# Kernel optimization log

Hardware: AMD Instinct MI355X
Metric: run time of the kernel (lower is better)

## Reference

```python
import jax, jax.numpy as jnp
import numpy as np

NUM_FIELDS = 16
EMBED = 256
BATCH = 2048
NUM_PAIRS = NUM_FIELDS * (NUM_FIELDS - 1) // 2  # 120


def setup_inputs() -> dict:
    key = jax.random.key(0)
    k1, k2, k3 = jax.random.split(key, 3)
    emb_inputs = jax.random.normal(k1, (BATCH, NUM_FIELDS, EMBED), dtype=jnp.float32)
    bound = 1.0 / np.sqrt(NUM_PAIRS)  # torch: 1/sqrt(weight.size(0)) = 1/sqrt(in_features)
    weight = jax.random.uniform(k2, (NUM_PAIRS, EMBED, EMBED), dtype=jnp.float32,
                                minval=-bound, maxval=bound)
    bias = jax.random.uniform(k3, (NUM_PAIRS, EMBED), dtype=jnp.float32,
                              minval=-bound, maxval=bound)
    return {"emb_inputs": emb_inputs, "weight": weight, "bias": bias}


def reference(emb_inputs, weight, bias):
    # Pair indices (i, j) with i < j over fields
    row_idx, col_idx = np.triu_indices(NUM_FIELDS, k=1)  # each length NUM_PAIRS
    p = emb_inputs[:, row_idx]  # (B, P, E)
    q = emb_inputs[:, col_idx]  # (B, P, E)
    # FieldEachTypeBilinear: (p @ W_p) * q + b_p, per-pair weight W_p (E, E)
    out = jnp.einsum('bpe,pef->bpf', p, weight) * q + bias  # (B, P, E)
    return out
```

## Files before the change

### kernel.cpp

```cpp
#include <hip/hip_runtime.h>
#include <hip/hip_bf16.h>
#include <stdint.h>

#define BATCH   2048
#define NF      16
#define EMBED   256
#define NPAIRS  120
#define OUTROW  (NPAIRS*EMBED)
#define EMBROW  (NF*EMBED)

typedef __attribute__((ext_vector_type(8))) __bf16 bf16x8;
typedef __attribute__((ext_vector_type(4))) float  f32x4;

typedef __attribute__((address_space(3))) void       lds_void;
typedef const __attribute__((address_space(1))) void g_void;

__device__ __forceinline__ unsigned short f2bf(float f) {
    unsigned u = __float_as_uint(f);
    u += 0x7FFF + ((u >> 16) & 1);
    return (unsigned short)(u >> 16);
}

__device__ __forceinline__ void pair_rc(int p, int& r, int& c) {
    int rr = 0, base = 0;
    while (p >= base + (NF - 1 - rr)) { base += NF - 1 - rr; ++rr; }
    r = rr; c = rr + 1 + (p - base);
}

__global__ __launch_bounds__(256) void emb_permute(const float* __restrict__ emb,
                                                   unsigned short* __restrict__ embp) {
    __shared__ float tile[64][65];
    const int b0 = blockIdx.x * 64;
    const int e0 = blockIdx.y * 64;
    const int f  = blockIdx.z;
    const int t  = threadIdx.x;
#pragma unroll
    for (int rnd = 0; rnd < 4; ++rnd) {
        int bl = rnd * 16 + (t >> 4);
        int el = (t & 15) * 4;
        const float4 v = *(const float4*)(emb + (size_t)(b0 + bl) * EMBROW + f * EMBED + e0 + el);
        tile[bl][el] = v.x; tile[bl][el + 1] = v.y; tile[bl][el + 2] = v.z; tile[bl][el + 3] = v.w;
    }
    __syncthreads();
#pragma unroll
    for (int rnd = 0; rnd < 2; ++rnd) {
        int ec = rnd * 4 + (t >> 6);
        int bl = t & 63;
        unsigned short h[8];
#pragma unroll
        for (int i = 0; i < 8; ++i) h[i] = f2bf(tile[bl][ec * 8 + i]);
        uint4 w;
        w.x = h[0] | ((unsigned)h[1] << 16);
        w.y = h[2] | ((unsigned)h[3] << 16);
        w.z = h[4] | ((unsigned)h[5] << 16);
        w.w = h[6] | ((unsigned)h[7] << 16);
        *(uint4*)(embp + (size_t)f * (32u * BATCH * 8) + (size_t)(e0 / 8 + ec) * (BATCH * 8)
                        + (size_t)(b0 + bl) * 8) = w;
    }
}

__global__ __launch_bounds__(256) void wt_permute(const float* __restrict__ wt,
                                                  unsigned short* __restrict__ wtp) {
    __shared__ float tile[64][65];
    const int e0 = blockIdx.x * 64;
    const int f0 = blockIdx.y * 64;
    const int p  = blockIdx.z;
    const int t  = threadIdx.x;
#pragma unroll
    for (int rnd = 0; rnd < 4; ++rnd) {
        int el = rnd * 16 + (t >> 4);
        int fl = (t & 15) * 4;
        const float4 v = *(const float4*)(wt + (size_t)p * (EMBED * EMBED) + (size_t)(e0 + el) * EMBED + f0 + fl);
        tile[el][fl] = v.x; tile[el][fl + 1] = v.y; tile[el][fl + 2] = v.z; tile[el][fl + 3] = v.w;
    }
    __syncthreads();
#pragma unroll
    for (int rnd = 0; rnd < 2; ++rnd) {
        int ec = rnd * 4 + (t >> 6);
        int fl = t & 63;
        unsigned short h[8];
#pragma unroll
        for (int i = 0; i < 8; ++i) h[i] = f2bf(tile[ec * 8 + i][fl]);
        uint4 w;
        w.x = h[0] | ((unsigned)h[1] << 16);
        w.y = h[2] | ((unsigned)h[3] << 16);
        w.z = h[4] | ((unsigned)h[5] << 16);
        w.w = h[6] | ((unsigned)h[7] << 16);
        *(uint4*)(wtp + (size_t)p * (EMBED * EMBED) + (size_t)(e0 / 8 + ec) * (EMBED * 8)
                       + (size_t)(f0 + fl) * 8) = w;
    }
}

__global__ __launch_bounds__(256, 4) void bilinear_main(
        const float* __restrict__ emb, const float* __restrict__ bias,
        const unsigned short* __restrict__ embp, const unsigned short* __restrict__ wtp,
        float* __restrict__ out) {
    __shared__ __align__(16) unsigned short s_lds[16384];
#define A_BUF(k) (s_lds + (k) * 4096)
#define B_BUF(k) (s_lds + 8192 + (k) * 4096)

    const int nblk = blockIdx.x, mblk = blockIdx.y, p = blockIdx.z;
    int r, c; pair_rc(p, r, c);
    const int m0 = mblk * 128, n0 = nblk * 128;
    const int t = threadIdx.x;
    const int wave = t >> 6, lane = t & 63;
    const int wm = (wave >> 1) * 64, wn = (wave & 1) * 64;
    const int kq = lane >> 4, l15 = lane & 15;

    const unsigned short* a_base = embp + (size_t)r * (32u * BATCH * 8);
    const unsigned short* b_base = wtp + (size_t)p * (EMBED * EMBED);

    f32x4 acc[4][4] = {};

#define STAGE(buf, ki)                                                              \
    {                                                                               \
        _Pragma("unroll")                                                           \
        for (int i = 0; i < 2; ++i) {                                               \
            int q  = i * 256 + t;                    \
            int kc = q >> 7, xl = q & 127;                                          \
            const unsigned short* ga = a_base + (size_t)((ki) * 4 + kc) * (BATCH * 8) \
                                             + (size_t)(m0 + xl) * 8;               \
            __builtin_amdgcn_global_load_lds((g_void*)ga,                           \
                (lds_void*)(A_BUF(buf) + q * 8), 16, 0, 0);                         \
            const unsigned short* gb = b_base + (size_t)((ki) * 4 + kc) * (EMBED * 8) \
                                             + (size_t)(n0 + xl) * 8;               \
            __builtin_amdgcn_global_load_lds((g_void*)gb,                           \
                (lds_void*)(B_BUF(buf) + q * 8), 16, 0, 0);                         \
        }                                                                           \
    }

#define COMPUTE(buf)                                                                \
    {                                                                               \
        bf16x8 af[4], bfr[4];                                                       \
        _Pragma("unroll")                                                           \
        for (int i = 0; i < 4; ++i)                                                 \
            af[i] = *(const bf16x8*)(A_BUF(buf) + (kq * 128 + wm + i * 16 + l15) * 8); \
        _Pragma("unroll")                                                           \
        for (int j = 0; j < 4; ++j)                                                 \
            bfr[j] = *(const bf16x8*)(B_BUF(buf) + (kq * 128 + wn + j * 16 + l15) * 8); \
        _Pragma("unroll")                                                           \
        for (int i = 0; i < 4; ++i)                                                 \
            _Pragma("unroll")                                                       \
            for (int j = 0; j < 4; ++j)                                             \
                acc[i][j] = __builtin_amdgcn_mfma_f32_16x16x32_bf16(af[i], bfr[j], acc[i][j], 0, 0, 0); \
    }

#define FENCE asm volatile("" ::: "memory")
#define SBAR  __builtin_amdgcn_sched_barrier(0)
#define BAR()                                                                       \
    {                                                                               \
        SBAR;                                                                       \
        asm volatile("s_waitcnt lgkmcnt(0)" ::: "memory");                          \
        SBAR;                                                                       \
        __builtin_amdgcn_s_barrier();                                               \
        SBAR;                                                                       \
    }
#define WAITVM(N)                                                                   \
    {                                                                               \
        SBAR;                                                                       \
        asm volatile("s_waitcnt vmcnt(" #N ")" ::: "memory");                       \
        SBAR;                                                                       \
    }

    STAGE(0, 0) FENCE; SBAR;
    STAGE(1, 1) FENCE; SBAR;

                WAITVM(4) BAR(); COMPUTE(0) BAR();
    STAGE(0, 2) WAITVM(4) BAR(); COMPUTE(1) BAR();
    STAGE(1, 3) WAITVM(4) BAR(); COMPUTE(0) BAR();
    STAGE(0, 4) WAITVM(4) BAR(); COMPUTE(1) BAR();
    STAGE(1, 5) WAITVM(4) BAR(); COMPUTE(0) BAR();
    STAGE(0, 6) WAITVM(4) BAR(); COMPUTE(1) BAR();
    STAGE(1, 7) WAITVM(4) BAR(); COMPUTE(0) BAR();
                WAITVM(0) BAR(); COMPUTE(1)

    __syncthreads();

    float* epw = (float*)s_lds + wave * (16 * 66);
    const int lrow4 = lane >> 4;
    const int lcol  = (lane & 15) * 4;
    const f32x4 bv = *(const f32x4*)(bias + p * EMBED + n0 + wn + lcol);

#pragma unroll
    for (int i = 0; i < 4; ++i) {
#pragma unroll
        for (int j = 0; j < 4; ++j)
#pragma unroll
            for (int reg = 0; reg < 4; ++reg)
                epw[(kq * 4 + reg) * 66 + j * 16 + l15] = acc[i][j][reg];
#pragma unroll
        for (int rr = 0; rr < 4; ++rr) {
            const int lrow = rr * 4 + lrow4;
            const f32x4 v = *(const f32x4*)&epw[lrow * 66 + lcol];
            const int row  = m0 + wm + i * 16 + lrow;
            const f32x4 q = *(const f32x4*)(emb + (size_t)row * EMBROW + c * EMBED + n0 + wn + lcol);
            f32x4 o = v * q + bv;
            __builtin_nontemporal_store(o, (f32x4*)(out + (size_t)row * OUTROW + p * EMBED + n0 + wn + lcol));
        }
    }
#undef STAGE
#undef COMPUTE
#undef FENCE
#undef SBAR
#undef BAR
#undef WAITVM
#undef A_BUF
#undef B_BUF
}

extern "C" void kernel_launch(void* const* d_in, const int* in_sizes, int n_in,
                              void* d_out, int out_size, void* d_ws, size_t ws_size,
                              hipStream_t stream) {
    const float* emb    = (const float*)d_in[0];
    const float* weight = (const float*)d_in[1];
    const float* bias   = (const float*)d_in[2];
    float* out = (float*)d_out;

    unsigned short* wtp  = (unsigned short*)d_ws;
    unsigned short* embp = (unsigned short*)((char*)d_ws + 15728640);

    wt_permute<<<dim3(4, 4, NPAIRS), 256, 0, stream>>>(weight, wtp);
    emb_permute<<<dim3(BATCH / 64, EMBED / 64, NF), 256, 0, stream>>>(emb, embp);
    bilinear_main<<<dim3(2, BATCH / 128, NPAIRS), 256, 0, stream>>>(emb, bias, embp, wtp, out);
}
```

Baseline: 346.1 us.

## Widen block tile to full N=256 with 8 waves and triple-buffered LDS

Each block now covers all 256 output columns of a pair for 128 batch rows, using 512 threads (8 waves). This removes the duplicate A-tile loads that two N-blocks used to make, and halves the grid. The K pipeline goes from double to triple buffering, so there are more loads in flight, with adjusted vmcnt waits. In exchange, LDS per block grows to about 72KB, which may lower occupancy, and the block count drops to 1920.

After: 341.1 us. Within noise of the previous version (-1.4%).

```diff
diff --git a/kernel.cpp b/kernel.cpp
--- a/kernel.cpp
+++ b/kernel.cpp
@@ -91,20 +91,21 @@
     }
 }
 
-__global__ __launch_bounds__(256, 4) void bilinear_main(
+__global__ __launch_bounds__(512, 4) void bilinear_main(
         const float* __restrict__ emb, const float* __restrict__ bias,
         const unsigned short* __restrict__ embp, const unsigned short* __restrict__ wtp,
         float* __restrict__ out) {
-    __shared__ __align__(16) unsigned short s_lds[16384];
+    __shared__ __align__(16) unsigned short s_lds[36864];
 #define A_BUF(k) (s_lds + (k) * 4096)
-#define B_BUF(k) (s_lds + 8192 + (k) * 4096)
-
-    const int nblk = blockIdx.x, mblk = blockIdx.y, p = blockIdx.z;
+#define B_BUF(k) (s_lds + 12288 + (k) * 8192)
+
+    const int mblk = blockIdx.x, p = blockIdx.y;
     int r, c; pair_rc(p, r, c);
-    const int m0 = mblk * 128, n0 = nblk * 128;
+    const int m0 = mblk * 128;
     const int t = threadIdx.x;
     const int wave = t >> 6, lane = t & 63;
-    const int wm = (wave >> 1) * 64, wn = (wave & 1) * 64;
+    const int wm = (wave >> 2) * 64;
+    const int wn = (wave & 3) * 64;
     const int kq = lane >> 4, l15 = lane & 15;
 
     const unsigned short* a_base = embp + (size_t)r * (32u * BATCH * 8);
@@ -114,18 +115,21 @@
 
 #define STAGE(buf, ki)                                                              \
     {                                                                               \
-        _Pragma("unroll")                                                           \
-        for (int i = 0; i < 2; ++i) {                                               \
-            int q  = i * 256 + t;                    \
-            int kc = q >> 7, xl = q & 127;                                          \
+        {                                                                           \
+            int kc = t >> 7, xl = t & 127;        \
             const unsigned short* ga = a_base + (size_t)((ki) * 4 + kc) * (BATCH * 8) \
                                              + (size_t)(m0 + xl) * 8;               \
             __builtin_amdgcn_global_load_lds((g_void*)ga,                           \
-                (lds_void*)(A_BUF(buf) + q * 8), 16, 0, 0);                         \
+                (lds_void*)(A_BUF(buf) + t * 8), 16, 0, 0);                         \
+        }                                                                           \
+        _Pragma("unroll")                                                           \
+        for (int i = 0; i < 2; ++i) {                                               \
+            int qb = i * 512 + t;                  \
+            int kc = qb >> 8, xl = qb & 255;                                        \
             const unsigned short* gb = b_base + (size_t)((ki) * 4 + kc) * (EMBED * 8) \
-                                             + (size_t)(n0 + xl) * 8;               \
+                                             + (size_t)xl * 8;                      \
             __builtin_amdgcn_global_load_lds((g_void*)gb,                           \
-                (lds_void*)(B_BUF(buf) + q * 8), 16, 0, 0);                         \
+                (lds_void*)(B_BUF(buf) + qb * 8), 16, 0, 0);                        \
         }                                                                           \
     }
 
@@ -137,7 +141,7 @@
             af[i] = *(const bf16x8*)(A_BUF(buf) + (kq * 128 + wm + i * 16 + l15) * 8); \
         _Pragma("unroll")                                                           \
         for (int j = 0; j < 4; ++j)                                                 \
-            bfr[j] = *(const bf16x8*)(B_BUF(buf) + (kq * 128 + wn + j * 16 + l15) * 8); \
+            bfr[j] = *(const bf16x8*)(B_BUF(buf) + (kq * 256 + wn + j * 16 + l15) * 8); \
         _Pragma("unroll")                                                           \
         for (int i = 0; i < 4; ++i)                                                 \
             _Pragma("unroll")                                                       \
@@ -164,14 +168,16 @@
 
     STAGE(0, 0) FENCE; SBAR;
     STAGE(1, 1) FENCE; SBAR;
-
-                WAITVM(4) BAR(); COMPUTE(0) BAR();
-    STAGE(0, 2) WAITVM(4) BAR(); COMPUTE(1) BAR();
-    STAGE(1, 3) WAITVM(4) BAR(); COMPUTE(0) BAR();
-    STAGE(0, 4) WAITVM(4) BAR(); COMPUTE(1) BAR();
-    STAGE(1, 5) WAITVM(4) BAR(); COMPUTE(0) BAR();
-    STAGE(0, 6) WAITVM(4) BAR(); COMPUTE(1) BAR();
-    STAGE(1, 7) WAITVM(4) BAR(); COMPUTE(0) BAR();
+    STAGE(2, 2) FENCE; SBAR;
+    WAITVM(0) BAR();
+
+                           COMPUTE(0) BAR();
+    STAGE(0, 3) WAITVM(6) BAR(); COMPUTE(1) BAR();
+    STAGE(1, 4) WAITVM(6) BAR(); COMPUTE(2) BAR();
+    STAGE(2, 5) WAITVM(6) BAR(); COMPUTE(0) BAR();
+    STAGE(0, 6) WAITVM(6) BAR(); COMPUTE(1) BAR();
+    STAGE(1, 7) WAITVM(6) BAR(); COMPUTE(2) BAR();
+                WAITVM(3) BAR(); COMPUTE(0) BAR();
                 WAITVM(0) BAR(); COMPUTE(1)
 
     __syncthreads();
@@ -179,7 +185,7 @@
     float* epw = (float*)s_lds + wave * (16 * 66);
     const int lrow4 = lane >> 4;
     const int lcol  = (lane & 15) * 4;
-    const f32x4 bv = *(const f32x4*)(bias + p * EMBED + n0 + wn + lcol);
+    const f32x4 bv = *(const f32x4*)(bias + p * EMBED + wn + lcol);
 
 #pragma unroll
     for (int i = 0; i < 4; ++i) {
@@ -193,9 +199,9 @@
             const int lrow = rr * 4 + lrow4;
             const f32x4 v = *(const f32x4*)&epw[lrow * 66 + lcol];
             const int row  = m0 + wm + i * 16 + lrow;
-            const f32x4 q = *(const f32x4*)(emb + (size_t)row * EMBROW + c * EMBED + n0 + wn + lcol);
+            const f32x4 q = *(const f32x4*)(emb + (size_t)row * EMBROW + c * EMBED + wn + lcol);
             f32x4 o = v * q + bv;
-            __builtin_nontemporal_store(o, (f32x4*)(out + (size_t)row * OUTROW + p * EMBED + n0 + wn + lcol));
+            __builtin_nontemporal_store(o, (f32x4*)(out + (size_t)row * OUTROW + p * EMBED + wn + lcol));
         }
     }
 #undef STAGE
@@ -221,5 +227,5 @@
 
     wt_permute<<<dim3(4, 4, NPAIRS), 256, 0, stream>>>(weight, wtp);
     emb_permute<<<dim3(BATCH / 64, EMBED / 64, NF), 256, 0, stream>>>(emb, embp);
-    bilinear_main<<<dim3(2, BATCH / 128, NPAIRS), 256, 0, stream>>>(emb, bias, embp, wtp, out);
-}
+    bilinear_main<<<dim3(BATCH / 128, NPAIRS), 512, 0, stream>>>(emb, bias, embp, wtp, out);
+}
```
